# Optimization experiments

Measured on AMD Instinct MI355X. Metric: run time of the kernel, lower is better.

Reference implementation:

```python
import jax, jax.numpy as jnp
import numpy as np

D_MODEL = 192
DEPTH = 16
D_INNER = 384   # expand=2
D_STATE = 16
D_CONV = 4
DT_RANK = 12    # ceil(192/16)
J = 42
T = 8
NUM_CLASSES = 1000
B = 64
EPS = 1e-5


def setup_inputs() -> dict:
    key = jax.random.key(0)
    ks = jax.random.split(key, 16)

    def n(k, shape, scale=0.02):
        return jax.random.normal(k, shape, jnp.float32) * scale

    dt_bias_init = float(np.log(np.expm1(0.01)))  # softplus^-1(0.01), mamba dt init
    A_init = jnp.log(jnp.tile(jnp.arange(1, D_STATE + 1, dtype=jnp.float32), (DEPTH, D_INNER, 1)))
    return {
        "x": jax.random.normal(ks[0], (B, T, J, 3), jnp.float32),
        "joint_embed_w": n(ks[1], (D_MODEL, 3)),
        "joint_embed_b": jnp.zeros((D_MODEL,), jnp.float32),
        "cls_token": n(ks[2], (1, 1, D_MODEL)),
        "spatial_pos": n(ks[3], (1, J + 1, D_MODEL)),
        "temporal_pos": n(ks[4], (1, T, D_MODEL)),
        "norm_w": jnp.ones((DEPTH, D_MODEL), jnp.float32),
        "in_proj_w": n(ks[5], (DEPTH, 2 * D_INNER, D_MODEL)),
        "conv_w": n(ks[6], (DEPTH, D_INNER, D_CONV), 0.1),
        "conv_b": jnp.zeros((DEPTH, D_INNER), jnp.float32),
        "x_proj_w": n(ks[7], (DEPTH, DT_RANK + 2 * D_STATE, D_INNER)),
        "dt_proj_w": n(ks[8], (DEPTH, D_INNER, DT_RANK), DT_RANK ** -0.5),
        "dt_proj_b": jnp.full((DEPTH, D_INNER), dt_bias_init, jnp.float32),
        "A_log": A_init,
        "Dp": jnp.ones((DEPTH, D_INNER), jnp.float32),
        "out_proj_w": n(ks[9], (DEPTH, D_MODEL, D_INNER)),
        "norm_f_w": jnp.ones((D_MODEL,), jnp.float32),
        "head_w": n(ks[10], (NUM_CLASSES, D_MODEL)),
        "head_b": jnp.zeros((NUM_CLASSES,), jnp.float32),
    }


def rmsnorm(x, w):
    return x * jax.lax.rsqrt(jnp.mean(x * x, axis=-1, keepdims=True) + EPS) * w


def mamba(x, in_w, cw, cb, xp_w, dtw, dtb, A_log, Dp, ow):
    # x: (B, L, d_model)
    Bsz, L, _ = x.shape
    xz = jnp.einsum('bld,ed->ble', x, in_w)          # (B,L,2*di)
    u, z = jnp.split(xz, 2, axis=-1)
    # depthwise causal conv over time
    uc = jnp.transpose(u, (0, 2, 1))                  # (B,di,L)
    uc = jnp.pad(uc, ((0, 0), (0, 0), (D_CONV - 1, 0)))
    uc = jax.lax.conv_general_dilated(
        uc, cw[:, None, :], (1,), 'VALID',
        dimension_numbers=('NCH', 'OIH', 'NCH'),
        feature_group_count=D_INNER) + cb[None, :, None]
    u = jax.nn.silu(jnp.transpose(uc, (0, 2, 1)))     # (B,L,di)
    dbl = jnp.einsum('bld,ed->ble', u, xp_w)          # (B,L,dt_rank+2*ds)
    dt, Bm, Cm = jnp.split(dbl, [DT_RANK, DT_RANK + D_STATE], axis=-1)
    delta = jax.nn.softplus(jnp.einsum('blr,dr->bld', dt, dtw) + dtb)  # (B,L,di)
    A = -jnp.exp(A_log)                               # (di,ds)

    def step(h, xs):
        d_t, B_t, C_t, u_t = xs                       # (B,di),(B,ds),(B,ds),(B,di)
        h = h * jnp.exp(d_t[..., None] * A) + (d_t * u_t)[..., None] * B_t[:, None, :]
        return h, jnp.einsum('bds,bs->bd', h, C_t)

    xs = (jnp.swapaxes(delta, 0, 1), jnp.swapaxes(Bm, 0, 1),
          jnp.swapaxes(Cm, 0, 1), jnp.swapaxes(u, 0, 1))
    h0 = jnp.zeros((Bsz, D_INNER, D_STATE), x.dtype)
    _, ys = jax.lax.scan(step, h0, xs)                # (L,B,di)
    y = jnp.swapaxes(ys, 0, 1) + u * Dp
    y = y * jax.nn.silu(z)
    return jnp.einsum('ble,de->bld', y, ow)


def reference(x, joint_embed_w, joint_embed_b, cls_token, spatial_pos, temporal_pos,
              norm_w, in_proj_w, conv_w, conv_b, x_proj_w, dt_proj_w, dt_proj_b,
              A_log, Dp, out_proj_w, norm_f_w, head_w, head_b):
    Bq, Tq, Jq, _ = x.shape
    xe = jnp.einsum('btjc,dc->btjd', x, joint_embed_w) + joint_embed_b
    xe = xe.reshape(Bq * Tq, Jq, D_MODEL)
    cls = jnp.broadcast_to(cls_token, (Bq * Tq, 1, D_MODEL))
    xcat = jnp.concatenate([cls, xe], axis=1) + spatial_pos   # (B*T, J+1, M)
    cls_tokens = xcat[:Bq, :1, :]
    body = xcat[:, 1:, :].reshape(Bq, Tq, Jq, D_MODEL)
    body = body.transpose(0, 2, 1, 3).reshape(Bq * Jq, Tq, D_MODEL) + temporal_pos
    body = body.reshape(Bq, Jq, Tq, D_MODEL).transpose(0, 2, 1, 3).reshape(Bq, Tq * Jq, D_MODEL)
    h = jnp.concatenate([cls_tokens, body], axis=1)           # (B, 1+T*J, M)

    residual = None
    for i in range(DEPTH):
        residual = h + residual if residual is not None else h
        hn = rmsnorm(residual, norm_w[i])
        h = mamba(hn, in_proj_w[i], conv_w[i], conv_b[i], x_proj_w[i],
                  dt_proj_w[i], dt_proj_b[i], A_log[i], Dp[i], out_proj_w[i])
    residual = h + residual
    feat = rmsnorm(residual, norm_f_w)[:, 0, :]
    return feat @ head_w.T + head_b
```

## Files before the change

### kernel.cpp

```cpp
#include <hip/hip_runtime.h>
#include <hip/hip_bf16.h>
#include <math.h>

#define B_ 64
#define T_ 8
#define J_ 42
#define L_ 337
#define D_ 192
#define E_ 384
#define S_ 16
#define R_ 12
#define DEPTH_ 16
#define NC_ 1000
#define M_ (B_*L_)
#define XZW_ (2*E_)
#define DBLW_ (R_+2*S_)
#define EPS_ 1e-5f
#define CH_ 16
#define NCH_ 22
#define EG_ (E_/8)
#define LOG2E_ 1.44269504088896f

typedef float    f32x4  __attribute__((ext_vector_type(4)));
typedef unsigned u32x4  __attribute__((ext_vector_type(4)));
typedef __bf16   bf16x8 __attribute__((ext_vector_type(8)));
typedef unsigned short ushort8 __attribute__((ext_vector_type(8)));

__device__ __forceinline__ float sigmoid_(float x){ return 1.f/(1.f+__expf(-x)); }
__device__ __forceinline__ float softplus_(float x){
  return (x > 20.f) ? x : __logf(1.f + __expf(x));
}
__device__ __forceinline__ unsigned short f2bf(float f){
  unsigned u = __float_as_uint(f);
  unsigned r = (u + 0x7fffu + ((u>>16)&1u)) >> 16;
  return (unsigned short)r;
}
__device__ __forceinline__ float bf2f(unsigned short h){
  return __uint_as_float(((unsigned)h)<<16);
}

__global__ void cvt_bf16_kernel(const float* __restrict__ in,
                                unsigned short* __restrict__ out, int n){
  int i = blockIdx.x*blockDim.x + threadIdx.x;
  if (i < n) out[i] = f2bf(in[i]);
}

__global__ void scan_prep_kernel(const float* __restrict__ dtw,
                                 const float* __restrict__ A_log,
                                 float* __restrict__ dtwT,
                                 float* __restrict__ a1v){
  int idx = blockIdx.x*blockDim.x + threadIdx.x;
  if (idx >= DEPTH_*E_) return;
  int d = idx % E_;
  int i = idx / E_;
  a1v[idx] = -__expf(A_log[((size_t)i*E_ + d)*S_]) * LOG2E_;
  #pragma unroll
  for (int r=0;r<R_;r++)
    dtwT[((size_t)i*R_ + r)*E_ + d] = dtw[((size_t)i*E_ + d)*R_ + r];
}

__global__ __launch_bounds__(64) void embed_norm0_kernel(
    const float* __restrict__ x,
    const float* __restrict__ jw,
    const float* __restrict__ jb,
    const float* __restrict__ cls,
    const float* __restrict__ sp,
    const float* __restrict__ tp,
    const float* __restrict__ w,
    float* __restrict__ res,
    unsigned short* __restrict__ hn) {
  const int m = blockIdx.x;
  const int lane = threadIdx.x;
  const int l = m % L_;
  const size_t base = (size_t)m*D_;
  float r[3]; float ss = 0.f;
  if (l == 0) {
    #pragma unroll
    for (int i=0;i<3;i++){
      int d = lane + i*64;
      r[i] = cls[d] + sp[d];
      ss += r[i]*r[i];
    }
  } else {
    const int lm = l-1, t = lm / J_, j = lm % J_;
    const int b = m / L_;
    const float* xp = x + ((size_t)((b*T_+t)*J_ + j))*3;
    const float x0 = xp[0], x1 = xp[1], x2 = xp[2];
    #pragma unroll
    for (int i=0;i<3;i++){
      int d = lane + i*64;
      r[i] = jb[d] + sp[(1+j)*D_+d] + tp[t*D_+d]
           + x0*jw[d*3+0] + x1*jw[d*3+1] + x2*jw[d*3+2];
      ss += r[i]*r[i];
    }
  }
  #pragma unroll
  for (int off=32; off>=1; off>>=1) ss += __shfl_xor(ss, off, 64);
  float sc = rsqrtf(ss*(1.f/(float)D_) + EPS_);
  #pragma unroll
  for (int i=0;i<3;i++){
    int d = lane + i*64;
    res[base+d] = r[i];
    hn[base+d] = f2bf(r[i]*sc*w[d]);
  }
}

__global__ __launch_bounds__(256) void gemm_in(
    const unsigned short* __restrict__ A,
    const unsigned short* __restrict__ W,
    unsigned short* __restrict__ u_raw,
    unsigned short* __restrict__ z)
{
  const int wave = threadIdx.x >> 6;
  const int lane = threadIdx.x & 63;
  const int row0 = blockIdx.x * 64;
  const int col0 = (blockIdx.y * 4 + wave) * 64;
  const int lr = lane & 15;
  const int lk = (lane >> 4) * 8;
  f32x4 acc[4][4] = {};
  for (int k0 = 0; k0 < D_; k0 += 32) {
    bf16x8 af[4], bfr[4];
    #pragma unroll
    for (int i=0;i<4;i++)
      af[i] = __builtin_bit_cast(bf16x8,
          *(const u32x4*)(A + (size_t)(row0 + i*16 + lr)*D_ + k0 + lk));
    #pragma unroll
    for (int j=0;j<4;j++)
      bfr[j] = __builtin_bit_cast(bf16x8,
          *(const u32x4*)(W + (size_t)(col0 + j*16 + lr)*D_ + k0 + lk));
    #pragma unroll
    for (int i=0;i<4;i++)
      #pragma unroll
      for (int j=0;j<4;j++)
        acc[i][j] = __builtin_amdgcn_mfma_f32_16x16x32_bf16(af[i], bfr[j], acc[i][j], 0, 0, 0);
  }
  const int ro = (lane >> 4) * 4;
  unsigned short* dst = (col0 < E_) ? u_raw : z;
  const int cbase = (col0 < E_) ? col0 : (col0 - E_);
  #pragma unroll
  for (int i=0;i<4;i++)
    #pragma unroll
    for (int j=0;j<4;j++){
      int col = cbase + j*16 + lr;
      #pragma unroll
      for (int r=0;r<4;r++){
        int row = row0 + i*16 + ro + r;
        dst[(size_t)row*E_ + col] = f2bf(acc[i][j][r]);
      }
    }
}

__global__ __launch_bounds__(256) void gemm_xp(
    const unsigned short* __restrict__ A,
    const unsigned short* __restrict__ W,
    float* __restrict__ C)
{
  const int wave = threadIdx.x >> 6;
  const int lane = threadIdx.x & 63;
  const int row0 = blockIdx.x * 64 + wave * 16;
  const int lr = lane & 15;
  const int lk = (lane >> 4) * 8;
  const bf16x8 bzero = __builtin_bit_cast(bf16x8, (u32x4)(0u));
  f32x4 acc[3] = {};
  for (int k0 = 0; k0 < E_; k0 += 32) {
    bf16x8 af = __builtin_bit_cast(bf16x8,
        *(const u32x4*)(A + (size_t)(row0 + lr)*E_ + k0 + lk));
    #pragma unroll
    for (int j=0;j<3;j++){
      int col = j*16 + lr;
      bf16x8 bfr = (col < DBLW_) ? __builtin_bit_cast(bf16x8,
          *(const u32x4*)(W + (size_t)col*E_ + k0 + lk)) : bzero;
      acc[j] = __builtin_amdgcn_mfma_f32_16x16x32_bf16(af, bfr, acc[j], 0, 0, 0);
    }
  }
  const int ro = (lane >> 4) * 4;
  #pragma unroll
  for (int j=0;j<3;j++){
    int col = j*16 + lr;
    if (col >= DBLW_) continue;
    #pragma unroll
    for (int r=0;r<4;r++){
      int row = row0 + ro + r;
      C[(size_t)row*DBLW_ + col] = acc[j][r];
    }
  }
}

__global__ __launch_bounds__(256) void conv_silu_kernel(
    const unsigned short* __restrict__ u_raw,
    const float* __restrict__ cw,
    const float* __restrict__ cb,
    unsigned short* __restrict__ u2) {
  int idx = blockIdx.x*blockDim.x + threadIdx.x;
  if (idx >= M_*EG_) return;
  const int g = idx % EG_;
  const int m = idx / EG_;
  const int l = m % L_;
  const int d0 = g*8;
  float4 wr[8];
  #pragma unroll
  for (int j=0;j<8;j++) wr[j] = *(const float4*)(cw + (size_t)(d0+j)*4);
  float acc[8];
  {
    float4 b0 = *(const float4*)(cb + d0);
    float4 b1 = *(const float4*)(cb + d0 + 4);
    acc[0]=b0.x; acc[1]=b0.y; acc[2]=b0.z; acc[3]=b0.w;
    acc[4]=b1.x; acc[5]=b1.y; acc[6]=b1.z; acc[7]=b1.w;
  }
  #pragma unroll
  for (int k=0;k<4;k++){
    const int lk = l + k - 3;
    if (lk < 0) continue;
    const ushort8 v = *(const ushort8*)(u_raw + (size_t)(m + k - 3)*E_ + d0);
    #pragma unroll
    for (int j=0;j<8;j++){
      float tap = (k==0)?wr[j].x:(k==1)?wr[j].y:(k==2)?wr[j].z:wr[j].w;
      acc[j] = fmaf(tap, bf2f(v[j]), acc[j]);
    }
  }
  ushort8 o;
  #pragma unroll
  for (int j=0;j<8;j++){
    float a = acc[j];
    o[j] = f2bf(a * sigmoid_(a));
  }
  *(ushort8*)(u2 + (size_t)m*E_ + d0) = o;
}

__global__ __launch_bounds__(128) void scan_partA(
    const float* __restrict__ dbl,
    const unsigned short* __restrict__ u2,
    const float* __restrict__ dtwT,
    const float* __restrict__ dtb,
    const float* __restrict__ a1v,
    unsigned short* __restrict__ part_h,
    float* __restrict__ part_sd)
{
  const int b = blockIdx.x;
  const int d = blockIdx.y*128 + threadIdx.x;
  const int c = blockIdx.z;
  float dtw_r[R_];
  #pragma unroll
  for (int r=0;r<R_;r++) dtw_r[r] = dtwT[r*E_+d];
  const float dtb_r = dtb[d];
  const float a1 = a1v[d];
  float h[S_];
  #pragma unroll
  for (int s=0;s<S_;s++) h[s] = 0.f;
  float sum_dl = 0.f;
  const size_t m0 = (size_t)b*L_ + (size_t)c*CH_;

  for (int t=0; t<CH_; ++t) {
    const float4* dr = (const float4*)(dbl + (m0+t)*DBLW_);
    float4 q0=dr[0],q1=dr[1],q2=dr[2],q3=dr[3],q4=dr[4],q5=dr[5],q6=dr[6];
    const float u_ = bf2f(u2[(m0+t)*E_ + d]);
    float s0 = fmaf(q0.y,dtw_r[1], q0.x*dtw_r[0]);
    s0 = fmaf(q0.z,dtw_r[2], s0); s0 = fmaf(q0.w,dtw_r[3], s0);
    float s1 = fmaf(q1.y,dtw_r[5], q1.x*dtw_r[4]);
    s1 = fmaf(q1.z,dtw_r[6], s1); s1 = fmaf(q1.w,dtw_r[7], s1);
    float s2 = fmaf(q2.y,dtw_r[9], fmaf(q2.x,dtw_r[8], dtb_r));
    s2 = fmaf(q2.z,dtw_r[10], s2); s2 = fmaf(q2.w,dtw_r[11], s2);
    float dtv = softplus_((s0+s1)+s2);
    sum_dl += dtv;
    const float du = dtv * u_;
    const float rr = exp2f(dtv * a1);
    const float rr2 = rr*rr, rr3 = rr2*rr, rr4 = rr2*rr2;
    float p0=rr, p1=rr2, p2=rr3, p3=rr4;
    h[0]=fmaf(h[0],p0,du*q3.x); h[1]=fmaf(h[1],p1,du*q3.y);
    h[2]=fmaf(h[2],p2,du*q3.z); h[3]=fmaf(h[3],p3,du*q3.w);
    p0*=rr4; p1*=rr4; p2*=rr4; p3*=rr4;
    h[4]=fmaf(h[4],p0,du*q4.x); h[5]=fmaf(h[5],p1,du*q4.y);
    h[6]=fmaf(h[6],p2,du*q4.z); h[7]=fmaf(h[7],p3,du*q4.w);
    p0*=rr4; p1*=rr4; p2*=rr4; p3*=rr4;
    h[8]=fmaf(h[8],p0,du*q5.x);  h[9]=fmaf(h[9],p1,du*q5.y);
    h[10]=fmaf(h[10],p2,du*q5.z); h[11]=fmaf(h[11],p3,du*q5.w);
    p0*=rr4; p1*=rr4; p2*=rr4; p3*=rr4;
    h[12]=fmaf(h[12],p0,du*q6.x); h[13]=fmaf(h[13],p1,du*q6.y);
    h[14]=fmaf(h[14],p2,du*q6.z); h[15]=fmaf(h[15],p3,du*q6.w);
  }
  const size_t pb = (size_t)b*NCH_ + c;
  #pragma unroll
  for (int s=0;s<S_;s++) part_h[(pb*S_ + s)*E_ + d] = f2bf(h[s]);
  part_sd[pb*E_ + d] = sum_dl;
}

__global__ __launch_bounds__(256) void scan_combine(
    unsigned short* __restrict__ part_h,
    const float* __restrict__ part_sd,
    const float* __restrict__ a1v)
{
  int idx = blockIdx.x*blockDim.x + threadIdx.x;
  const int d = idx % E_;
  const int s = (idx / E_) % S_;
  const int b = idx / (E_*S_);
  const float a1s = a1v[d] * (float)(s+1);
  float hprev = 0.f;
  for (int c=0; c<NCH_-1; ++c) {
    const size_t off = (((size_t)b*NCH_ + c)*S_ + s)*E_ + d;
    const float tmp = bf2f(part_h[off]);
    part_h[off] = f2bf(hprev);
    const float sd = part_sd[((size_t)b*NCH_ + c)*E_ + d];
    hprev = fmaf(hprev, exp2f(a1s*sd), tmp);
  }
  part_h[(((size_t)b*NCH_ + NCH_-1)*S_ + s)*E_ + d] = f2bf(hprev);
}

__global__ __launch_bounds__(128) void scan_partC(
    const float* __restrict__ dbl,
    const unsigned short* __restrict__ u2,
    const unsigned short* __restrict__ zbuf,
    const float* __restrict__ dtwT, const float* __restrict__ dtb,
    const float* __restrict__ a1v, const float* __restrict__ Dp,
    const unsigned short* __restrict__ part_h,
    unsigned short* __restrict__ y)
{
  const int b = blockIdx.x;
  const int d = blockIdx.y*128 + threadIdx.x;
  const int c = blockIdx.z;
  const int t0 = c*CH_;
  const int nt = (t0 + CH_ <= L_) ? CH_ : (L_ - t0);
  float dtw_r[R_];
  #pragma unroll
  for (int r=0;r<R_;r++) dtw_r[r] = dtwT[r*E_+d];
  const float dtb_r = dtb[d];
  const float dpv   = Dp[d];
  const float a1 = a1v[d];
  float h[S_];
  {
    const size_t pb = (size_t)b*NCH_ + c;
    #pragma unroll
    for (int s=0;s<S_;s++) h[s] = bf2f(part_h[(pb*S_ + s)*E_ + d]);
  }
  const size_t m0 = (size_t)b*L_ + t0;

  for (int t=0; t<nt; ++t) {
    const float4* dr = (const float4*)(dbl + (m0+t)*DBLW_);
    float4 q0=dr[0],q1=dr[1],q2=dr[2],q3=dr[3],q4=dr[4],q5=dr[5],
           q6=dr[6],q7=dr[7],q8=dr[8],q9=dr[9],q10=dr[10];
    const float u_ = bf2f(u2[(m0+t)*E_ + d]);
    const float z_ = bf2f(zbuf[(m0+t)*E_ + d]);
    float s0 = fmaf(q0.y,dtw_r[1], q0.x*dtw_r[0]);
    s0 = fmaf(q0.z,dtw_r[2], s0); s0 = fmaf(q0.w,dtw_r[3], s0);
    float s1 = fmaf(q1.y,dtw_r[5], q1.x*dtw_r[4]);
    s1 = fmaf(q1.z,dtw_r[6], s1); s1 = fmaf(q1.w,dtw_r[7], s1);
    float s2 = fmaf(q2.y,dtw_r[9], fmaf(q2.x,dtw_r[8], dtb_r));
    s2 = fmaf(q2.z,dtw_r[10], s2); s2 = fmaf(q2.w,dtw_r[11], s2);
    float dtv = softplus_((s0+s1)+s2);
    const float du = dtv * u_;
    const float rr = exp2f(dtv * a1);
    const float rr2 = rr*rr, rr3 = rr2*rr, rr4 = rr2*rr2;
    float p0=rr, p1=rr2, p2=rr3, p3=rr4;
    float a0,a1_,a2,a3;
    h[0]=fmaf(h[0],p0,du*q3.x); a0=h[0]*q7.x;
    h[1]=fmaf(h[1],p1,du*q3.y); a1_=h[1]*q7.y;
    h[2]=fmaf(h[2],p2,du*q3.z); a2=h[2]*q7.z;
    h[3]=fmaf(h[3],p3,du*q3.w); a3=h[3]*q7.w;
    p0*=rr4; p1*=rr4; p2*=rr4; p3*=rr4;
    h[4]=fmaf(h[4],p0,du*q4.x); a0=fmaf(h[4],q8.x,a0);
    h[5]=fmaf(h[5],p1,du*q4.y); a1_=fmaf(h[5],q8.y,a1_);
    h[6]=fmaf(h[6],p2,du*q4.z); a2=fmaf(h[6],q8.z,a2);
    h[7]=fmaf(h[7],p3,du*q4.w); a3=fmaf(h[7],q8.w,a3);
    p0*=rr4; p1*=rr4; p2*=rr4; p3*=rr4;
    h[8]=fmaf(h[8],p0,du*q5.x);  a0=fmaf(h[8],q9.x,a0);
    h[9]=fmaf(h[9],p1,du*q5.y);  a1_=fmaf(h[9],q9.y,a1_);
    h[10]=fmaf(h[10],p2,du*q5.z); a2=fmaf(h[10],q9.z,a2);
    h[11]=fmaf(h[11],p3,du*q5.w); a3=fmaf(h[11],q9.w,a3);
    p0*=rr4; p1*=rr4; p2*=rr4; p3*=rr4;
    h[12]=fmaf(h[12],p0,du*q6.x); a0=fmaf(h[12],q10.x,a0);
    h[13]=fmaf(h[13],p1,du*q6.y); a1_=fmaf(h[13],q10.y,a1_);
    h[14]=fmaf(h[14],p2,du*q6.z); a2=fmaf(h[14],q10.z,a2);
    h[15]=fmaf(h[15],p3,du*q6.w); a3=fmaf(h[15],q10.w,a3);
    const float accv = (a0+a1_)+(a2+a3);
    const float yv = fmaf(u_, dpv, accv) * (z_ * sigmoid_(z_));
    y[(m0+t)*E_ + d] = f2bf(yv);
  }
}

__global__ __launch_bounds__(192) void gemm_out_fused(
    const unsigned short* __restrict__ A,
    const unsigned short* __restrict__ W,
    float* __restrict__ residual,
    const float* __restrict__ wnext,
    unsigned short* __restrict__ hn)
{
  const int wave = threadIdx.x >> 6;
  const int lane = threadIdx.x & 63;
  const int row0 = blockIdx.x * 64;
  const int col0 = wave * 64;
  const int lr = lane & 15;
  const int lk = (lane >> 4) * 8;
  f32x4 acc[4][4] = {};
  for (int k0 = 0; k0 < E_; k0 += 32) {
    bf16x8 af[4], bfr[4];
    #pragma unroll
    for (int i=0;i<4;i++)
      af[i] = __builtin_bit_cast(bf16x8,
          *(const u32x4*)(A + (size_t)(row0 + i*16 + lr)*E_ + k0 + lk));
    #pragma unroll
    for (int j=0;j<4;j++)
      bfr[j] = __builtin_bit_cast(bf16x8,
          *(const u32x4*)(W + (size_t)(col0 + j*16 + lr)*E_ + k0 + lk));
    #pragma unroll
    for (int i=0;i<4;i++)
      #pragma unroll
      for (int j=0;j<4;j++)
        acc[i][j] = __builtin_amdgcn_mfma_f32_16x16x32_bf16(af[i], bfr[j], acc[i][j], 0, 0, 0);
  }
  const int ro = (lane >> 4) * 4;
  __shared__ float rs[3][64];
  float wn[4];
  #pragma unroll
  for (int j=0;j<4;j++) wn[j] = wnext[col0 + j*16 + lr];
  #pragma unroll
  for (int i=0;i<4;i++){
    #pragma unroll
    for (int r=0;r<4;r++){
      int row = row0 + i*16 + ro + r;
      float psum = 0.f;
      #pragma unroll
      for (int j=0;j<4;j++){
        int col = col0 + j*16 + lr;
        float v = residual[(size_t)row*D_ + col] + acc[i][j][r];
        acc[i][j][r] = v;
        residual[(size_t)row*D_ + col] = v;
        psum = fmaf(v, v, psum);
      }
      psum += __shfl_xor(psum, 1);
      psum += __shfl_xor(psum, 2);
      psum += __shfl_xor(psum, 4);
      psum += __shfl_xor(psum, 8);
      if (lr == 0) rs[wave][i*16 + ro + r] = psum;
    }
  }
  __syncthreads();
  #pragma unroll
  for (int i=0;i<4;i++){
    #pragma unroll
    for (int r=0;r<4;r++){
      int rloc = i*16 + ro + r;
      float tot = rs[0][rloc] + rs[1][rloc] + rs[2][rloc];
      float sc = rsqrtf(tot*(1.f/(float)D_) + EPS_);
      int row = row0 + rloc;
      #pragma unroll
      for (int j=0;j<4;j++){
        int col = col0 + j*16 + lr;
        hn[(size_t)row*D_ + col] = f2bf(acc[i][j][r]*sc*wn[j]);
      }
    }
  }
}

__global__ __launch_bounds__(256) void final_head_kernel(
    const float* __restrict__ residual, const float* __restrict__ w,
    const float* __restrict__ hw, const float* __restrict__ hb,
    float* __restrict__ out) {
  __shared__ float fs[D_];
  __shared__ float red[4];
  const int b = blockIdx.x;
  const int tid = threadIdx.x;
  const size_t base = (size_t)b*L_*D_;
  float v = (tid < D_) ? residual[base+tid] : 0.f;
  float ss = v*v;
  #pragma unroll
  for (int off=32; off>=1; off>>=1) ss += __shfl_xor(ss, off, 64);
  if ((tid & 63) == 0) red[tid>>6] = ss;
  __syncthreads();
  const float tot = red[0]+red[1]+red[2]+red[3];
  const float sc = rsqrtf(tot*(1.f/(float)D_) + EPS_);
  if (tid < D_) fs[tid] = v*sc*w[tid];
  __syncthreads();
  for (int n=tid;n<NC_;n+=256){
    float acc = hb[n];
    #pragma unroll 4
    for (int k=0;k<D_;k++) acc += fs[k]*hw[(size_t)n*D_+k];
    out[(size_t)b*NC_+n] = acc;
  }
}

extern "C" void kernel_launch(void* const* d_in, const int* in_sizes, int n_in,
                              void* d_out, int out_size, void* d_ws, size_t ws_size,
                              hipStream_t stream) {
  const float* x        = (const float*)d_in[0];
  const float* jw       = (const float*)d_in[1];
  const float* jb       = (const float*)d_in[2];
  const float* cls      = (const float*)d_in[3];
  const float* sp       = (const float*)d_in[4];
  const float* tp       = (const float*)d_in[5];
  const float* norm_w   = (const float*)d_in[6];
  const float* in_w     = (const float*)d_in[7];
  const float* conv_w   = (const float*)d_in[8];
  const float* conv_b   = (const float*)d_in[9];
  const float* xp_w     = (const float*)d_in[10];
  const float* dt_w     = (const float*)d_in[11];
  const float* dt_b     = (const float*)d_in[12];
  const float* A_log    = (const float*)d_in[13];
  const float* Dp       = (const float*)d_in[14];
  const float* out_w    = (const float*)d_in[15];
  const float* norm_f_w = (const float*)d_in[16];
  const float* head_w   = (const float*)d_in[17];
  const float* head_b   = (const float*)d_in[18];
  float* out = (float*)d_out;

  float* ws = (float*)d_ws;
  float* residual = ws;
  float* dbl      = residual + (size_t)M_*D_;
  float* part_sd  = dbl      + (size_t)M_*DBLW_;
  float* dtwT     = part_sd  + (size_t)B_*NCH_*E_;
  float* a1v      = dtwT     + (size_t)DEPTH_*R_*E_;
  unsigned short* bw = (unsigned short*)(a1v + (size_t)DEPTH_*E_);
  unsigned short* hn     = bw;
  unsigned short* u_raw  = hn     + (size_t)M_*D_;
  unsigned short* zbuf   = u_raw  + (size_t)M_*E_;
  unsigned short* u2     = zbuf   + (size_t)M_*E_;
  unsigned short* ybuf   = u2     + (size_t)M_*E_;
  unsigned short* part_h = ybuf   + (size_t)M_*E_;
  unsigned short* w_in   = part_h + (size_t)B_*NCH_*S_*E_;
  unsigned short* w_xp   = w_in   + (size_t)DEPTH_*XZW_*D_;
  unsigned short* w_out  = w_xp   + (size_t)DEPTH_*DBLW_*E_;

  {
    int n1 = DEPTH_*XZW_*D_;
    int n2 = DEPTH_*DBLW_*E_;
    int n3 = DEPTH_*D_*E_;
    cvt_bf16_kernel<<<(n1+255)/256, 256, 0, stream>>>(in_w,  w_in,  n1);
    cvt_bf16_kernel<<<(n2+255)/256, 256, 0, stream>>>(xp_w,  w_xp,  n2);
    cvt_bf16_kernel<<<(n3+255)/256, 256, 0, stream>>>(out_w, w_out, n3);
    scan_prep_kernel<<<(DEPTH_*E_+255)/256, 256, 0, stream>>>(dt_w, A_log, dtwT, a1v);
  }

  embed_norm0_kernel<<<M_, 64, 0, stream>>>(x, jw, jb, cls, sp, tp, norm_w,
                                            residual, hn);

  for (int i = 0; i < DEPTH_; ++i) {
    gemm_in<<<dim3(M_/64, XZW_/256), 256, 0, stream>>>(
        hn, w_in + (size_t)i*XZW_*D_, u_raw, zbuf);
    conv_silu_kernel<<<(M_*EG_+255)/256, 256, 0, stream>>>(
        u_raw, conv_w + (size_t)i*E_*4, conv_b + (size_t)i*E_, u2);
    gemm_xp<<<M_/64, 256, 0, stream>>>(
        u2, w_xp + (size_t)i*DBLW_*E_, dbl);
    scan_partA<<<dim3(B_, E_/128, NCH_-1), 128, 0, stream>>>(
        dbl, u2, dtwT + (size_t)i*R_*E_, dt_b + (size_t)i*E_,
        a1v + (size_t)i*E_, part_h, part_sd);
    scan_combine<<<(B_*S_*E_)/256, 256, 0, stream>>>(
        part_h, part_sd, a1v + (size_t)i*E_);
    scan_partC<<<dim3(B_, E_/128, NCH_), 128, 0, stream>>>(
        dbl, u2, zbuf, dtwT + (size_t)i*R_*E_, dt_b + (size_t)i*E_,
        a1v + (size_t)i*E_, Dp + (size_t)i*E_, part_h, ybuf);
    const float* wnext = (i+1 < DEPTH_) ? (norm_w + (size_t)(i+1)*D_) : norm_f_w;
    gemm_out_fused<<<M_/64, 192, 0, stream>>>(
        ybuf, w_out + (size_t)i*D_*E_, residual, wnext, hn);
  }

  final_head_kernel<<<B_, 256, 0, stream>>>(residual, norm_f_w, head_w, head_b, out);
}
```

Before: 2.711 ms.

## Process two channels per thread in scan kernels to reuse dbl row loads

Both chunked scan kernels now have each thread handle two inner channels (d and d+192) in 192-thread blocks covering all 384 channels, instead of one channel per thread in 128-thread blocks. Each dbl row (dt, B, C values) is then loaded once per block rather than three times, and each thread gets two independent recurrences for more instruction-level parallelism. In exchange the block count drops threefold and register pressure roughly doubles, which may lower occupancy.

```diff
diff --git a/kernel.cpp b/kernel.cpp
--- a/kernel.cpp
+++ b/kernel.cpp
@@ -227,7 +227,7 @@
   *(ushort8*)(u2 + (size_t)m*E_ + d0) = o;
 }
 
-__global__ __launch_bounds__(128) void scan_partA(
+__global__ __launch_bounds__(192) void scan_partA(
     const float* __restrict__ dbl,
     const unsigned short* __restrict__ u2,
     const float* __restrict__ dtwT,
@@ -237,51 +237,57 @@
     float* __restrict__ part_sd)
 {
   const int b = blockIdx.x;
-  const int d = blockIdx.y*128 + threadIdx.x;
-  const int c = blockIdx.z;
-  float dtw_r[R_];
-  #pragma unroll
-  for (int r=0;r<R_;r++) dtw_r[r] = dtwT[r*E_+d];
-  const float dtb_r = dtb[d];
-  const float a1 = a1v[d];
-  float h[S_];
-  #pragma unroll
-  for (int s=0;s<S_;s++) h[s] = 0.f;
-  float sum_dl = 0.f;
+  const int c = blockIdx.y;
+  const int d0 = threadIdx.x;
+  const int d1 = threadIdx.x + 192;
+  float dtw[2][R_];
+  #pragma unroll
+  for (int r=0;r<R_;r++){ dtw[0][r]=dtwT[r*E_+d0]; dtw[1][r]=dtwT[r*E_+d1]; }
+  const float dtbv[2] = { dtb[d0], dtb[d1] };
+  const float a1c[2]  = { a1v[d0], a1v[d1] };
+  float h[2][S_] = {};
+  float sd[2] = {0.f, 0.f};
   const size_t m0 = (size_t)b*L_ + (size_t)c*CH_;
 
   for (int t=0; t<CH_; ++t) {
     const float4* dr = (const float4*)(dbl + (m0+t)*DBLW_);
     float4 q0=dr[0],q1=dr[1],q2=dr[2],q3=dr[3],q4=dr[4],q5=dr[5],q6=dr[6];
-    const float u_ = bf2f(u2[(m0+t)*E_ + d]);
-    float s0 = fmaf(q0.y,dtw_r[1], q0.x*dtw_r[0]);
-    s0 = fmaf(q0.z,dtw_r[2], s0); s0 = fmaf(q0.w,dtw_r[3], s0);
-    float s1 = fmaf(q1.y,dtw_r[5], q1.x*dtw_r[4]);
-    s1 = fmaf(q1.z,dtw_r[6], s1); s1 = fmaf(q1.w,dtw_r[7], s1);
-    float s2 = fmaf(q2.y,dtw_r[9], fmaf(q2.x,dtw_r[8], dtb_r));
-    s2 = fmaf(q2.z,dtw_r[10], s2); s2 = fmaf(q2.w,dtw_r[11], s2);
-    float dtv = softplus_((s0+s1)+s2);
-    sum_dl += dtv;
-    const float du = dtv * u_;
-    const float rr = exp2f(dtv * a1);
-    const float rr2 = rr*rr, rr3 = rr2*rr, rr4 = rr2*rr2;
-    float p0=rr, p1=rr2, p2=rr3, p3=rr4;
-    h[0]=fmaf(h[0],p0,du*q3.x); h[1]=fmaf(h[1],p1,du*q3.y);
-    h[2]=fmaf(h[2],p2,du*q3.z); h[3]=fmaf(h[3],p3,du*q3.w);
-    p0*=rr4; p1*=rr4; p2*=rr4; p3*=rr4;
-    h[4]=fmaf(h[4],p0,du*q4.x); h[5]=fmaf(h[5],p1,du*q4.y);
-    h[6]=fmaf(h[6],p2,du*q4.z); h[7]=fmaf(h[7],p3,du*q4.w);
-    p0*=rr4; p1*=rr4; p2*=rr4; p3*=rr4;
-    h[8]=fmaf(h[8],p0,du*q5.x);  h[9]=fmaf(h[9],p1,du*q5.y);
-    h[10]=fmaf(h[10],p2,du*q5.z); h[11]=fmaf(h[11],p3,du*q5.w);
-    p0*=rr4; p1*=rr4; p2*=rr4; p3*=rr4;
-    h[12]=fmaf(h[12],p0,du*q6.x); h[13]=fmaf(h[13],p1,du*q6.y);
-    h[14]=fmaf(h[14],p2,du*q6.z); h[15]=fmaf(h[15],p3,du*q6.w);
+    const float uv[2] = { bf2f(u2[(m0+t)*E_+d0]), bf2f(u2[(m0+t)*E_+d1]) };
+    #pragma unroll
+    for (int ch=0; ch<2; ++ch){
+      float s0 = fmaf(q0.y,dtw[ch][1], q0.x*dtw[ch][0]);
+      s0 = fmaf(q0.z,dtw[ch][2], s0); s0 = fmaf(q0.w,dtw[ch][3], s0);
+      float s1 = fmaf(q1.y,dtw[ch][5], q1.x*dtw[ch][4]);
+      s1 = fmaf(q1.z,dtw[ch][6], s1); s1 = fmaf(q1.w,dtw[ch][7], s1);
+      float s2 = fmaf(q2.y,dtw[ch][9], fmaf(q2.x,dtw[ch][8], dtbv[ch]));
+      s2 = fmaf(q2.z,dtw[ch][10], s2); s2 = fmaf(q2.w,dtw[ch][11], s2);
+      float dtv = softplus_((s0+s1)+s2);
+      sd[ch] += dtv;
+      const float du = dtv * uv[ch];
+      const float rr = exp2f(dtv * a1c[ch]);
+      const float rr2 = rr*rr, rr3 = rr2*rr, rr4 = rr2*rr2;
+      float p0=rr, p1=rr2, p2=rr3, p3=rr4;
+      h[ch][0]=fmaf(h[ch][0],p0,du*q3.x); h[ch][1]=fmaf(h[ch][1],p1,du*q3.y);
+      h[ch][2]=fmaf(h[ch][2],p2,du*q3.z); h[ch][3]=fmaf(h[ch][3],p3,du*q3.w);
+      p0*=rr4; p1*=rr4; p2*=rr4; p3*=rr4;
+      h[ch][4]=fmaf(h[ch][4],p0,du*q4.x); h[ch][5]=fmaf(h[ch][5],p1,du*q4.y);
+      h[ch][6]=fmaf(h[ch][6],p2,du*q4.z); h[ch][7]=fmaf(h[ch][7],p3,du*q4.w);
+      p0*=rr4; p1*=rr4; p2*=rr4; p3*=rr4;
+      h[ch][8]=fmaf(h[ch][8],p0,du*q5.x);  h[ch][9]=fmaf(h[ch][9],p1,du*q5.y);
+      h[ch][10]=fmaf(h[ch][10],p2,du*q5.z); h[ch][11]=fmaf(h[ch][11],p3,du*q5.w);
+      p0*=rr4; p1*=rr4; p2*=rr4; p3*=rr4;
+      h[ch][12]=fmaf(h[ch][12],p0,du*q6.x); h[ch][13]=fmaf(h[ch][13],p1,du*q6.y);
+      h[ch][14]=fmaf(h[ch][14],p2,du*q6.z); h[ch][15]=fmaf(h[ch][15],p3,du*q6.w);
+    }
   }
   const size_t pb = (size_t)b*NCH_ + c;
   #pragma unroll
-  for (int s=0;s<S_;s++) part_h[(pb*S_ + s)*E_ + d] = f2bf(h[s]);
-  part_sd[pb*E_ + d] = sum_dl;
+  for (int s=0;s<S_;s++){
+    part_h[(pb*S_ + s)*E_ + d0] = f2bf(h[0][s]);
+    part_h[(pb*S_ + s)*E_ + d1] = f2bf(h[1][s]);
+  }
+  part_sd[pb*E_ + d0] = sd[0];
+  part_sd[pb*E_ + d1] = sd[1];
 }
 
 __global__ __launch_bounds__(256) void scan_combine(
@@ -305,7 +311,7 @@
   part_h[(((size_t)b*NCH_ + NCH_-1)*S_ + s)*E_ + d] = f2bf(hprev);
 }
 
-__global__ __launch_bounds__(128) void scan_partC(
+__global__ __launch_bounds__(192) void scan_partC(
     const float* __restrict__ dbl,
     const unsigned short* __restrict__ u2,
     const unsigned short* __restrict__ zbuf,
@@ -315,21 +321,25 @@
     unsigned short* __restrict__ y)
 {
   const int b = blockIdx.x;
-  const int d = blockIdx.y*128 + threadIdx.x;
-  const int c = blockIdx.z;
+  const int c = blockIdx.y;
   const int t0 = c*CH_;
   const int nt = (t0 + CH_ <= L_) ? CH_ : (L_ - t0);
-  float dtw_r[R_];
-  #pragma unroll
-  for (int r=0;r<R_;r++) dtw_r[r] = dtwT[r*E_+d];
-  const float dtb_r = dtb[d];
-  const float dpv   = Dp[d];
-  const float a1 = a1v[d];
-  float h[S_];
+  const int d0 = threadIdx.x;
+  const int d1 = threadIdx.x + 192;
+  float dtw[2][R_];
+  #pragma unroll
+  for (int r=0;r<R_;r++){ dtw[0][r]=dtwT[r*E_+d0]; dtw[1][r]=dtwT[r*E_+d1]; }
+  const float dtbv[2] = { dtb[d0], dtb[d1] };
+  const float a1c[2]  = { a1v[d0], a1v[d1] };
+  const float dpv[2]  = { Dp[d0], Dp[d1] };
+  float h[2][S_];
   {
     const size_t pb = (size_t)b*NCH_ + c;
     #pragma unroll
-    for (int s=0;s<S_;s++) h[s] = bf2f(part_h[(pb*S_ + s)*E_ + d]);
+    for (int s=0;s<S_;s++){
+      h[0][s] = bf2f(part_h[(pb*S_ + s)*E_ + d0]);
+      h[1][s] = bf2f(part_h[(pb*S_ + s)*E_ + d1]);
+    }
   }
   const size_t m0 = (size_t)b*L_ + t0;
 
@@ -337,42 +347,45 @@
     const float4* dr = (const float4*)(dbl + (m0+t)*DBLW_);
     float4 q0=dr[0],q1=dr[1],q2=dr[2],q3=dr[3],q4=dr[4],q5=dr[5],
            q6=dr[6],q7=dr[7],q8=dr[8],q9=dr[9],q10=dr[10];
-    const float u_ = bf2f(u2[(m0+t)*E_ + d]);
-    const float z_ = bf2f(zbuf[(m0+t)*E_ + d]);
-    float s0 = fmaf(q0.y,dtw_r[1], q0.x*dtw_r[0]);
-    s0 = fmaf(q0.z,dtw_r[2], s0); s0 = fmaf(q0.w,dtw_r[3], s0);
-    float s1 = fmaf(q1.y,dtw_r[5], q1.x*dtw_r[4]);
-    s1 = fmaf(q1.z,dtw_r[6], s1); s1 = fmaf(q1.w,dtw_r[7], s1);
-    float s2 = fmaf(q2.y,dtw_r[9], fmaf(q2.x,dtw_r[8], dtb_r));
-    s2 = fmaf(q2.z,dtw_r[10], s2); s2 = fmaf(q2.w,dtw_r[11], s2);
-    float dtv = softplus_((s0+s1)+s2);
-    const float du = dtv * u_;
-    const float rr = exp2f(dtv * a1);
-    const float rr2 = rr*rr, rr3 = rr2*rr, rr4 = rr2*rr2;
-    float p0=rr, p1=rr2, p2=rr3, p3=rr4;
-    float a0,a1_,a2,a3;
-    h[0]=fmaf(h[0],p0,du*q3.x); a0=h[0]*q7.x;
-    h[1]=fmaf(h[1],p1,du*q3.y); a1_=h[1]*q7.y;
-    h[2]=fmaf(h[2],p2,du*q3.z); a2=h[2]*q7.z;
-    h[3]=fmaf(h[3],p3,du*q3.w); a3=h[3]*q7.w;
-    p0*=rr4; p1*=rr4; p2*=rr4; p3*=rr4;
-    h[4]=fmaf(h[4],p0,du*q4.x); a0=fmaf(h[4],q8.x,a0);
-    h[5]=fmaf(h[5],p1,du*q4.y); a1_=fmaf(h[5],q8.y,a1_);
-    h[6]=fmaf(h[6],p2,du*q4.z); a2=fmaf(h[6],q8.z,a2);
-    h[7]=fmaf(h[7],p3,du*q4.w); a3=fmaf(h[7],q8.w,a3);
-    p0*=rr4; p1*=rr4; p2*=rr4; p3*=rr4;
-    h[8]=fmaf(h[8],p0,du*q5.x);  a0=fmaf(h[8],q9.x,a0);
-    h[9]=fmaf(h[9],p1,du*q5.y);  a1_=fmaf(h[9],q9.y,a1_);
-    h[10]=fmaf(h[10],p2,du*q5.z); a2=fmaf(h[10],q9.z,a2);
-    h[11]=fmaf(h[11],p3,du*q5.w); a3=fmaf(h[11],q9.w,a3);
-    p0*=rr4; p1*=rr4; p2*=rr4; p3*=rr4;
-    h[12]=fmaf(h[12],p0,du*q6.x); a0=fmaf(h[12],q10.x,a0);
-    h[13]=fmaf(h[13],p1,du*q6.y); a1_=fmaf(h[13],q10.y,a1_);
-    h[14]=fmaf(h[14],p2,du*q6.z); a2=fmaf(h[14],q10.z,a2);
-    h[15]=fmaf(h[15],p3,du*q6.w); a3=fmaf(h[15],q10.w,a3);
-    const float accv = (a0+a1_)+(a2+a3);
-    const float yv = fmaf(u_, dpv, accv) * (z_ * sigmoid_(z_));
-    y[(m0+t)*E_ + d] = f2bf(yv);
+    const float uv[2] = { bf2f(u2[(m0+t)*E_+d0]), bf2f(u2[(m0+t)*E_+d1]) };
+    const float zv[2] = { bf2f(zbuf[(m0+t)*E_+d0]), bf2f(zbuf[(m0+t)*E_+d1]) };
+    #pragma unroll
+    for (int ch=0; ch<2; ++ch){
+      float s0 = fmaf(q0.y,dtw[ch][1], q0.x*dtw[ch][0]);
+      s0 = fmaf(q0.z,dtw[ch][2], s0); s0 = fmaf(q0.w,dtw[ch][3], s0);
+      float s1 = fmaf(q1.y,dtw[ch][5], q1.x*dtw[ch][4]);
+      s1 = fmaf(q1.z,dtw[ch][6], s1); s1 = fmaf(q1.w,dtw[ch][7], s1);
+      float s2 = fmaf(q2.y,dtw[ch][9], fmaf(q2.x,dtw[ch][8], dtbv[ch]));
+      s2 = fmaf(q2.z,dtw[ch][10], s2); s2 = fmaf(q2.w,dtw[ch][11], s2);
+      float dtv = softplus_((s0+s1)+s2);
+      const float du = dtv * uv[ch];
+      const float rr = exp2f(dtv * a1c[ch]);
+      const float rr2 = rr*rr, rr3 = rr2*rr, rr4 = rr2*rr2;
+      float p0=rr, p1=rr2, p2=rr3, p3=rr4;
+      float a0,a1_,a2,a3;
+      h[ch][0]=fmaf(h[ch][0],p0,du*q3.x); a0=h[ch][0]*q7.x;
+      h[ch][1]=fmaf(h[ch][1],p1,du*q3.y); a1_=h[ch][1]*q7.y;
+      h[ch][2]=fmaf(h[ch][2],p2,du*q3.z); a2=h[ch][2]*q7.z;
+      h[ch][3]=fmaf(h[ch][3],p3,du*q3.w); a3=h[ch][3]*q7.w;
+      p0*=rr4; p1*=rr4; p2*=rr4; p3*=rr4;
+      h[ch][4]=fmaf(h[ch][4],p0,du*q4.x); a0=fmaf(h[ch][4],q8.x,a0);
+      h[ch][5]=fmaf(h[ch][5],p1,du*q4.y); a1_=fmaf(h[ch][5],q8.y,a1_);
+      h[ch][6]=fmaf(h[ch][6],p2,du*q4.z); a2=fmaf(h[ch][6],q8.z,a2);
+      h[ch][7]=fmaf(h[ch][7],p3,du*q4.w); a3=fmaf(h[ch][7],q8.w,a3);
+      p0*=rr4; p1*=rr4; p2*=rr4; p3*=rr4;
+      h[ch][8]=fmaf(h[ch][8],p0,du*q5.x);  a0=fmaf(h[ch][8],q9.x,a0);
+      h[ch][9]=fmaf(h[ch][9],p1,du*q5.y);  a1_=fmaf(h[ch][9],q9.y,a1_);
+      h[ch][10]=fmaf(h[ch][10],p2,du*q5.z); a2=fmaf(h[ch][10],q9.z,a2);
+      h[ch][11]=fmaf(h[ch][11],p3,du*q5.w); a3=fmaf(h[ch][11],q9.w,a3);
+      p0*=rr4; p1*=rr4; p2*=rr4; p3*=rr4;
+      h[ch][12]=fmaf(h[ch][12],p0,du*q6.x); a0=fmaf(h[ch][12],q10.x,a0);
+      h[ch][13]=fmaf(h[ch][13],p1,du*q6.y); a1_=fmaf(h[ch][13],q10.y,a1_);
+      h[ch][14]=fmaf(h[ch][14],p2,du*q6.z); a2=fmaf(h[ch][14],q10.z,a2);
+      h[ch][15]=fmaf(h[ch][15],p3,du*q6.w); a3=fmaf(h[ch][15],q10.w,a3);
+      const float accv = (a0+a1_)+(a2+a3);
+      const float yv = fmaf(uv[ch], dpv[ch], accv) * (zv[ch] * sigmoid_(zv[ch]));
+      y[(m0+t)*E_ + (ch ? d1 : d0)] = f2bf(yv);
+    }
   }
 }
 
@@ -538,12 +551,12 @@
         u_raw, conv_w + (size_t)i*E_*4, conv_b + (size_t)i*E_, u2);
     gemm_xp<<<M_/64, 256, 0, stream>>>(
         u2, w_xp + (size_t)i*DBLW_*E_, dbl);
-    scan_partA<<<dim3(B_, E_/128, NCH_-1), 128, 0, stream>>>(
+    scan_partA<<<dim3(B_, NCH_-1), 192, 0, stream>>>(
         dbl, u2, dtwT + (size_t)i*R_*E_, dt_b + (size_t)i*E_,
         a1v + (size_t)i*E_, part_h, part_sd);
     scan_combine<<<(B_*S_*E_)/256, 256, 0, stream>>>(
         part_h, part_sd, a1v + (size_t)i*E_);
-    scan_partC<<<dim3(B_, E_/128, NCH_), 128, 0, stream>>>(
+    scan_partC<<<dim3(B_, NCH_), 192, 0, stream>>>(
         dbl, u2, zbuf, dtwT + (size_t)i*R_*E_, dt_b + (size_t)i*E_,
         a1v + (size_t)i*E_, Dp + (size_t)i*E_, part_h, ybuf);
     const float* wnext = (i+1 < DEPTH_) ? (norm_w + (size_t)(i+1)*D_) : norm_f_w;
```

Measured after the change: 2.874 ms. 6.0% more time.
